# Kernel tuning notes

Hardware: AMD Instinct MI355X
Metric: run time of the kernel (lower is better)

## Reference

```python
import math
import jax, jax.numpy as jnp
import numpy as np

D_MODEL = 512
N_HEADS = 8
HD = D_MODEL // N_HEADS  # 64
RATIO = 8      # csa_compress_ratio
STRIDE = 4     # csa_compress_stride
WINDOW = 128   # csa_window_size
THETA = 10000.0


def _rope_freqs(L):
    half = HD // 2
    inv_freq = 1.0 / (THETA ** (jnp.arange(half, dtype=jnp.float32) / half))
    t = jnp.arange(L, dtype=jnp.float32)
    f = t[:, None] * inv_freq[None, :]  # [L, half]
    return jnp.cos(f), jnp.sin(f)


def _apply_rope(x, cos, sin):
    # x: [B, H, L, hd]
    half = x.shape[-1] // 2
    x1, x2 = x[..., :half], x[..., half:]
    cos = cos[None, None]
    sin = sin[None, None]
    return jnp.concatenate([x1 * cos - x2 * sin, x1 * sin + x2 * cos], axis=-1)


def setup_inputs() -> dict:
    key = jax.random.key(0)
    ks = jax.random.split(key, 9)
    B, L, D = 2, 2048, D_MODEL
    s = 0.02
    return {
        "x": jax.random.normal(ks[0], (B, L, D), dtype=jnp.float32),
        "wq": jax.random.normal(ks[1], (D, D), dtype=jnp.float32) * s,
        "wk": jax.random.normal(ks[2], (D, D), dtype=jnp.float32) * s,
        "wv": jax.random.normal(ks[3], (D, D), dtype=jnp.float32) * s,
        "wo": jax.random.normal(ks[4], (D, D), dtype=jnp.float32) * s,
        "wk_c": jax.random.normal(ks[5], (D, D), dtype=jnp.float32) * s,
        "wv_c": jax.random.normal(ks[6], (D, D), dtype=jnp.float32) * s,
        "gate_logits": jax.random.normal(ks[7], (RATIO,), dtype=jnp.float32) * s,
        "sink_logit": jnp.zeros((N_HEADS, 1), dtype=jnp.float32),
    }


def reference(x, wq, wk, wv, wo, wk_c, wv_c, gate_logits, sink_logit):
    B, L, D = x.shape
    f32 = jnp.float32

    def heads(t):  # [B,L,D] -> [B,H,L,hd]
        return t.reshape(B, L, N_HEADS, HD).transpose(0, 2, 1, 3)

    q = heads(x @ wq.T)
    k = heads(x @ wk.T)
    v = heads(x @ wv.T)

    cos, sin = _rope_freqs(L)
    q = _apply_rope(q.astype(f32), cos, sin).astype(x.dtype)
    k = _apply_rope(k.astype(f32), cos, sin).astype(x.dtype)

    # --- KV compression: strided overlapping windows, learned gate pooling ---
    n_windows = max(1, (L - RATIO) // STRIDE + 1)
    idx = jnp.clip(
        jnp.arange(RATIO)[None, :] + jnp.arange(n_windows)[:, None] * STRIDE, 0, L - 1
    )  # [Lc, ratio]
    windows = x[:, idx, :]  # [B, Lc, ratio, D]
    gate_w = jax.nn.softmax(gate_logits)
    x_c = jnp.einsum("bwrd,r->bwd", windows, gate_w)  # [B, Lc, D]
    Lc = n_windows

    k_c = x_c @ wk_c.T
    v_c = x_c @ wv_c.T
    k_c = k_c.reshape(B, Lc, N_HEADS, HD).transpose(0, 2, 1, 3)
    v_c = v_c.reshape(B, Lc, N_HEADS, HD).transpose(0, 2, 1, 3)

    scale = math.sqrt(HD)
    pos = jnp.arange(L)

    # compressed branch: causal on compressed-entry end positions
    comp_scores = jnp.einsum("bhqd,bhkd->bhqk", q, k_c) / scale  # [B,H,L,Lc]
    entry_end = jnp.arange(Lc) * STRIDE + RATIO - 1
    causal_c = pos[:, None] >= entry_end[None, :]
    comp_scores = jnp.where(causal_c[None, None], comp_scores, -jnp.inf)

    # local window branch: causal band of width WINDOW
    win_scores = jnp.einsum("bhqd,bhkd->bhqk", q, k) / scale  # [B,H,L,L]
    dist = pos[:, None] - pos[None, :]
    win_mask = (dist >= 0) & (dist < WINDOW)
    win_scores = jnp.where(win_mask[None, None], win_scores, -jnp.inf)

    sink = jnp.broadcast_to(sink_logit[None, :, None, :], (B, N_HEADS, L, 1))

    all_scores = jnp.concatenate(
        [comp_scores.astype(f32), win_scores.astype(f32), sink.astype(f32)], axis=-1
    )
    attn = jax.nn.softmax(all_scores, axis=-1).astype(x.dtype)

    w_comp = attn[..., :Lc]
    w_win = attn[..., Lc:Lc + L]
    out = jnp.einsum("bhqk,bhkd->bhqd", w_comp, v_c) + jnp.einsum(
        "bhqk,bhkd->bhqd", w_win, v
    )
    out = out.transpose(0, 2, 1, 3).reshape(B, L, D)
    return out @ wo.T
```

## Files before the change

kernel.cpp:

```cpp
#include <hip/hip_runtime.h>
#include <hip/hip_bf16.h>
#include <cmath>

#define BATCH 2
#define LSEQ 2048
#define DMODEL 512
#define NHEADS 8
#define HD 64
#define RATIO 8
#define STRIDE 4
#define WINDOW 128
#define LC 511

typedef short short8 __attribute__((ext_vector_type(8)));
typedef float floatx4 __attribute__((ext_vector_type(4)));

__device__ inline unsigned short f2bf(float f) {
  unsigned u = __float_as_uint(f);
  u += 0x7FFFu + ((u >> 16) & 1u);
  return (unsigned short)(u >> 16);
}

__device__ inline void gld_lds16(const unsigned short* g, short* l) {
  __builtin_amdgcn_global_load_lds(
      (const __attribute__((address_space(1))) unsigned int*)g,
      (__attribute__((address_space(3))) unsigned int*)l, 16, 0, 0);
}

__global__ void conv_all(const float* __restrict__ x,
                         const float* __restrict__ w0, const float* __restrict__ w1,
                         const float* __restrict__ w2, const float* __restrict__ w3,
                         const float* __restrict__ w4, const float* __restrict__ w5,
                         const float* __restrict__ gate,
                         unsigned short* __restrict__ xb,
                         unsigned short* __restrict__ wqkvb,
                         unsigned short* __restrict__ wkvcb,
                         unsigned short* __restrict__ wob,
                         unsigned short* __restrict__ xcb,
                         float2* __restrict__ cstab) {
  int idx = blockIdx.x * blockDim.x + threadIdx.x;
  if (idx < 917504) {
    const float* src;
    unsigned short* dst;
    int off;
    if (idx < 524288) {
      src = x; dst = xb; off = idx;
    } else {
      int r = idx - 524288;
      int wi = r >> 16;
      off = r & 65535;
      switch (wi) {
        case 0: src = w0; dst = wqkvb; break;
        case 1: src = w1; dst = wqkvb + 4 * 65536; break;
        case 2: src = w2; dst = wqkvb + 8 * 65536; break;
        case 3: src = w3; dst = wkvcb; break;
        case 4: src = w4; dst = wkvcb + 4 * 65536; break;
        default: src = w5; dst = wob; break;
      }
    }
    float4 v = ((const float4*)src)[off];
    ushort4 o;
    o.x = f2bf(v.x); o.y = f2bf(v.y); o.z = f2bf(v.z); o.w = f2bf(v.w);
    ((ushort4*)dst)[off] = o;
  } else if (idx < 1048320) {
    int r = idx - 917504;
    int d4 = r & 127;
    int t = r >> 7;
    int w = t % LC;
    int b = t / LC;
    float g[8];
    float m = -1e30f;
#pragma unroll
    for (int i = 0; i < 8; ++i) { g[i] = gate[i]; m = fmaxf(m, g[i]); }
    float ssum = 0.f;
#pragma unroll
    for (int i = 0; i < 8; ++i) { g[i] = __expf(g[i] - m); ssum += g[i]; }
    float inv = 1.f / ssum;
    const float* xb4 = x + ((size_t)(b * LSEQ + w * STRIDE)) * DMODEL + d4 * 4;
    float4 acc = make_float4(0.f, 0.f, 0.f, 0.f);
#pragma unroll
    for (int i = 0; i < 8; ++i) {
      float4 v = *(const float4*)(xb4 + (size_t)i * DMODEL);
      acc.x += g[i] * v.x; acc.y += g[i] * v.y;
      acc.z += g[i] * v.z; acc.w += g[i] * v.w;
    }
    ushort4 o;
    o.x = f2bf(acc.x * inv); o.y = f2bf(acc.y * inv);
    o.z = f2bf(acc.z * inv); o.w = f2bf(acc.w * inv);
    ((ushort4*)xcb)[(size_t)(b * LC + w) * 128 + d4] = o;
  } else {
    int e = idx - 1048320;
    int p = e >> 5, j = e & 31;
    float inv_freq = __expf(-(float)j * (9.210340371976184f / 32.f));
    float s, c;
    sincosf((float)p * inv_freq, &s, &c);
    cstab[e] = make_float2(c, s);
  }
}

__global__ __launch_bounds__(256) void proj_gemm(
    const unsigned short* __restrict__ xb, const unsigned short* __restrict__ xcb,
    const unsigned short* __restrict__ wqkvb, const unsigned short* __restrict__ wkvcb,
    const float2* __restrict__ cstab,
    unsigned short* __restrict__ qbuf, unsigned short* __restrict__ kbuf,
    unsigned short* __restrict__ vbuf, unsigned short* __restrict__ kcb,
    unsigned short* __restrict__ vcb) {
  __shared__ short As[128 * 64];
  __shared__ short Bs[128 * 64];
  const int tid = threadIdx.x;
  const int w = tid >> 6, l = tid & 63;
  const int lr = l & 15, lg = l >> 4;

  const int bid = blockIdx.x;
  const bool qkv = (bid < 384);
  const unsigned short* Ap;
  const unsigned short* Bp;
  int bm, bn, Am1;
  if (qkv) {
    Ap = xb; Bp = wqkvb; bm = (bid & 31) * 128; bn = (bid >> 5) * 128; Am1 = 4095;
  } else {
    int r = bid - 384;
    Ap = xcb; Bp = wkvcb; bm = (r & 7) * 128; bn = (r >> 3) * 128; Am1 = 1021;
  }
  const int wm = (w >> 1) * 64, wn = (w & 1) * 64;

  floatx4 acc[4][4];
#pragma unroll
  for (int i = 0; i < 4; ++i)
#pragma unroll
    for (int j = 0; j < 4; ++j) acc[i][j] = 0.f;

  const int trow = tid >> 3;
  const int cs = (tid & 7) ^ (trow & 7);
  size_t aoffs[4];
#pragma unroll
  for (int i = 0; i < 4; ++i) {
    int ar = bm + trow + i * 32;
    if (ar > Am1) ar = Am1;
    aoffs[i] = (size_t)ar * DMODEL + cs * 8;
  }
  const size_t boff = (size_t)(bn + trow) * DMODEL + cs * 8;
  const int ldsbase = (tid & 192) * 8;

  for (int k0 = 0; k0 < DMODEL; k0 += 64) {
    __syncthreads();
#pragma unroll
    for (int i = 0; i < 4; ++i) {
      gld_lds16(Ap + aoffs[i] + k0, As + i * 2048 + ldsbase);
      gld_lds16(Bp + boff + (size_t)i * 32 * DMODEL + k0, Bs + i * 2048 + ldsbase);
    }
    __syncthreads();

#pragma unroll
    for (int kk = 0; kk < 2; ++kk) {
      const int kc16 = kk * 4 + lg;
      short8 a[4], bf[4];
#pragma unroll
      for (int mi = 0; mi < 4; ++mi) {
        int r = wm + mi * 16 + lr;
        a[mi] = *(const short8*)&As[r * 64 + ((kc16 ^ (r & 7)) * 8)];
      }
#pragma unroll
      for (int nj = 0; nj < 4; ++nj) {
        int r = wn + nj * 16 + lr;
        bf[nj] = *(const short8*)&Bs[r * 64 + ((kc16 ^ (r & 7)) * 8)];
      }
#pragma unroll
      for (int mi = 0; mi < 4; ++mi)
#pragma unroll
        for (int nj = 0; nj < 4; ++nj)
          acc[mi][nj] = __builtin_amdgcn_mfma_f32_16x16x32_bf16(
              a[mi], bf[nj], acc[mi][nj], 0, 0, 0);
    }
  }

  if (qkv) {
    if (bn < 1024) {
      unsigned short* dst = (bn < 512) ? qbuf : kbuf;
      const int cbase = (bn + wn) & 511;
#pragma unroll
      for (int mi = 0; mi < 4; ++mi) {
#pragma unroll
        for (int i = 0; i < 4; ++i) {
          int row = bm + wm + mi * 16 + lg * 4 + i;
          int p = row & 2047;
#pragma unroll
          for (int nj = 0; nj < 2; ++nj) {
            float2 cssin = cstab[p * 32 + nj * 16 + lr];
            float a = acc[mi][nj][i], b2 = acc[mi][nj + 2][i];
            int cc = cbase + nj * 16 + lr;
            dst[(size_t)row * 512 + cc] = f2bf(a * cssin.x - b2 * cssin.y);
            dst[(size_t)row * 512 + cc + 32] = f2bf(a * cssin.y + b2 * cssin.x);
          }
        }
      }
    } else {
#pragma unroll
      for (int mi = 0; mi < 4; ++mi) {
#pragma unroll
        for (int i = 0; i < 4; ++i) {
          int row = bm + wm + mi * 16 + lg * 4 + i;
#pragma unroll
          for (int nj = 0; nj < 4; ++nj) {
            int col = bn + wn + nj * 16 + lr - 1024;
            vbuf[(size_t)row * 512 + col] = f2bf(acc[mi][nj][i]);
          }
        }
      }
    }
  } else {
    unsigned short* dst = ((bn + wn) < 512) ? kcb : vcb;
    const int cbase = (bn + wn) & 511;
#pragma unroll
    for (int mi = 0; mi < 4; ++mi) {
#pragma unroll
      for (int i = 0; i < 4; ++i) {
        int row = bm + wm + mi * 16 + lg * 4 + i;
        if (row < 1022) {
#pragma unroll
          for (int nj = 0; nj < 4; ++nj)
            dst[(size_t)row * 512 + cbase + nj * 16 + lr] = f2bf(acc[mi][nj][i]);
        }
      }
    }
  }
}

__global__ __launch_bounds__(256) void wo_gemm(
    const unsigned short* __restrict__ A, const unsigned short* __restrict__ B,
    float* __restrict__ C) {
  __shared__ short As[128 * 64];
  __shared__ short Bs[64 * 64];
  const int tid = threadIdx.x;
  const int w = tid >> 6, l = tid & 63;
  const int lr = l & 15, lg = l >> 4;
  const int bm = blockIdx.x * 128, bn = blockIdx.y * 64;
  const int wm = (w >> 1) * 64, wn = (w & 1) * 32;

  floatx4 acc[4][2];
#pragma unroll
  for (int i = 0; i < 4; ++i)
#pragma unroll
    for (int j = 0; j < 2; ++j) acc[i][j] = 0.f;

  const int trow = tid >> 3;
  const int cs = (tid & 7) ^ (trow & 7);
  const size_t aoff = (size_t)(bm + trow) * DMODEL + cs * 8;
  const size_t boff = (size_t)(bn + trow) * DMODEL + cs * 8;
  const int ldsbase = (tid & 192) * 8;

  for (int k0 = 0; k0 < DMODEL; k0 += 64) {
    __syncthreads();
#pragma unroll
    for (int i = 0; i < 4; ++i)
      gld_lds16(A + aoff + (size_t)i * 32 * DMODEL + k0, As + i * 2048 + ldsbase);
#pragma unroll
    for (int i = 0; i < 2; ++i)
      gld_lds16(B + boff + (size_t)i * 32 * DMODEL + k0, Bs + i * 2048 + ldsbase);
    __syncthreads();

#pragma unroll
    for (int kk = 0; kk < 2; ++kk) {
      const int kc16 = kk * 4 + lg;
      short8 a[4], bf[2];
#pragma unroll
      for (int mi = 0; mi < 4; ++mi) {
        int r = wm + mi * 16 + lr;
        a[mi] = *(const short8*)&As[r * 64 + ((kc16 ^ (r & 7)) * 8)];
      }
#pragma unroll
      for (int nj = 0; nj < 2; ++nj) {
        int r = wn + nj * 16 + lr;
        bf[nj] = *(const short8*)&Bs[r * 64 + ((kc16 ^ (r & 7)) * 8)];
      }
#pragma unroll
      for (int mi = 0; mi < 4; ++mi)
#pragma unroll
        for (int nj = 0; nj < 2; ++nj)
          acc[mi][nj] = __builtin_amdgcn_mfma_f32_16x16x32_bf16(
              a[mi], bf[nj], acc[mi][nj], 0, 0, 0);
    }
  }

#pragma unroll
  for (int mi = 0; mi < 4; ++mi) {
#pragma unroll
    for (int i = 0; i < 4; ++i) {
      int row = bm + wm + mi * 16 + lg * 4 + i;
#pragma unroll
      for (int nj = 0; nj < 2; ++nj)
        C[(size_t)row * 512 + bn + wn + nj * 16 + lr] = acc[mi][nj][i];
    }
  }
}

__global__ __launch_bounds__(256, 2) void attn_kernel(
    const unsigned short* __restrict__ qb, const unsigned short* __restrict__ kb,
    const unsigned short* __restrict__ vb, const unsigned short* __restrict__ kcb,
    const unsigned short* __restrict__ vcb, const float* __restrict__ sink,
    unsigned short* __restrict__ ob) {
  __shared__ short Ks[2][64][72];
  __shared__ short Vt[2][64][72];
  __shared__ short Pl[4][16][72];

  const int n = blockIdx.x;
  const int b = n >> 8;
  const int mm = n & 255;
  const int h = mm >> 5;
  int qt = mm & 31;
  if (b) qt = 31 - qt;
  const int q0 = qt * 64;
  const int tid = threadIdx.x;
  const int w = tid >> 6, l = tid & 63;
  const int lr = l & 15, lg = l >> 4;
  const int hoff = h * HD;

  short8 Qa0, Qa1;
  {
    const unsigned short* qrow =
        qb + ((size_t)(b * LSEQ + q0 + w * 16 + lr)) * DMODEL + hoff;
    Qa0 = *(const short8*)(qrow + lg * 8);
    Qa1 = *(const short8*)(qrow + 32 + lg * 8);
  }

  floatx4 Oacc[4];
#pragma unroll
  for (int f = 0; f < 4; ++f) Oacc[f] = 0.f;
  float mrow[4] = {-3.0e38f, -3.0e38f, -3.0e38f, -3.0e38f};
  float lrow[4] = {0.f, 0.f, 0.f, 0.f};

  int ncm = q0 / 4 + 15;
  if (ncm > LC) ncm = LC;
  const int ntc = (ncm + 63) >> 6;
  const int w0 = (q0 > 127) ? (q0 - 127) : 0;
  const int ntw = (q0 + 64 - w0 + 63) >> 6;
  const int ntt = ntc + ntw;

  const int skey = tid >> 2, sd = (tid & 3) * 16;
  const int vkey = (tid & 31) * 2, vd = (tid >> 5) * 8;

  short8 kreg0, kreg1, vreg0, vreg1;

  auto load_tile = [&](int tt) {
    const bool isC = (tt < ntc);
    const int tbase = isC ? tt * 64 : (w0 + (tt - ntc) * 64);
    const unsigned short* Kp = isC ? kcb : kb;
    const unsigned short* Vp = isC ? vcb : vb;
    const int rmax = isC ? (LC - 1) : (LSEQ - 1);
    const size_t brow = isC ? (size_t)(b * LC) : (size_t)(b * LSEQ);
    int kr = tbase + skey;      if (kr > rmax) kr = rmax;
    int vr0 = tbase + vkey;     if (vr0 > rmax) vr0 = rmax;
    int vr1 = tbase + vkey + 1; if (vr1 > rmax) vr1 = rmax;
    const unsigned short* src = Kp + (brow + kr) * DMODEL + hoff + sd;
    kreg0 = *(const short8*)(src);
    kreg1 = *(const short8*)(src + 8);
    vreg0 = *(const short8*)(Vp + (brow + vr0) * DMODEL + hoff + vd);
    vreg1 = *(const short8*)(Vp + (brow + vr1) * DMODEL + hoff + vd);
  };
  auto store_tile = [&](int bsel) {
    *(short8*)&Ks[bsel][skey][sd] = kreg0;
    *(short8*)&Ks[bsel][skey][sd + 8] = kreg1;
#pragma unroll
    for (int j = 0; j < 8; ++j) {
      unsigned pk = (unsigned)(unsigned short)vreg0[j] |
                    ((unsigned)(unsigned short)vreg1[j] << 16);
      *(unsigned*)&Vt[bsel][vd + j][vkey] = pk;
    }
  };

  load_tile(0);

  for (int tt = 0; tt < ntt; ++tt) {
    const int bsel = tt & 1;
    store_tile(bsel);
    if (tt + 1 < ntt) load_tile(tt + 1);
    __syncthreads();

    const bool isC = (tt < ntc);
    const int tbase = isC ? tt * 64 : (w0 + (tt - ntc) * 64);

    floatx4 S[4];
    __builtin_amdgcn_s_setprio(1);
#pragma unroll
    for (int f = 0; f < 4; ++f) {
      floatx4 acc = 0.f;
      short8 kf0 = *(const short8*)&Ks[bsel][f * 16 + lr][lg * 8];
      short8 kf1 = *(const short8*)&Ks[bsel][f * 16 + lr][32 + lg * 8];
      acc = __builtin_amdgcn_mfma_f32_16x16x32_bf16(Qa0, kf0, acc, 0, 0, 0);
      acc = __builtin_amdgcn_mfma_f32_16x16x32_bf16(Qa1, kf1, acc, 0, 0, 0);
      S[f] = acc;
    }
    __builtin_amdgcn_s_setprio(0);

    float tmax[4] = {-3.0e38f, -3.0e38f, -3.0e38f, -3.0e38f};
#pragma unroll
    for (int f = 0; f < 4; ++f) {
      const int key = tbase + f * 16 + lr;
#pragma unroll
      for (int i = 0; i < 4; ++i) {
        const int p = q0 + w * 16 + lg * 4 + i;
        bool valid;
        if (isC) valid = (key <= LC - 1) && (p >= key * 4 + 7);
        else     valid = (p >= key) && (p - key < WINDOW);
        float s = valid ? S[f][i] * 0.125f : -3.0e38f;
        S[f][i] = s;
        tmax[i] = fmaxf(tmax[i], s);
      }
    }
#pragma unroll
    for (int i = 0; i < 4; ++i) {
      tmax[i] = fmaxf(tmax[i], __shfl_xor(tmax[i], 1));
      tmax[i] = fmaxf(tmax[i], __shfl_xor(tmax[i], 2));
      tmax[i] = fmaxf(tmax[i], __shfl_xor(tmax[i], 4));
      tmax[i] = fmaxf(tmax[i], __shfl_xor(tmax[i], 8));
    }
    float r[4];
#pragma unroll
    for (int i = 0; i < 4; ++i) {
      float mn = fmaxf(mrow[i], tmax[i]);
      r[i] = __expf(mrow[i] - mn);
      mrow[i] = mn;
    }
#pragma unroll
    for (int f = 0; f < 4; ++f) {
#pragma unroll
      for (int i = 0; i < 4; ++i) Oacc[f][i] *= r[i];
    }
    float lsum[4] = {0.f, 0.f, 0.f, 0.f};
#pragma unroll
    for (int f = 0; f < 4; ++f) {
#pragma unroll
      for (int i = 0; i < 4; ++i) {
        float ee = (S[f][i] > -1.0e38f) ? __expf(S[f][i] - mrow[i]) : 0.f;
        lsum[i] += ee;
        Pl[w][lg * 4 + i][f * 16 + lr] = (short)f2bf(ee);
      }
    }
#pragma unroll
    for (int i = 0; i < 4; ++i) {
      float t = lsum[i];
      t += __shfl_xor(t, 1); t += __shfl_xor(t, 2);
      t += __shfl_xor(t, 4); t += __shfl_xor(t, 8);
      lrow[i] = lrow[i] * r[i] + t;
    }
    asm volatile("s_waitcnt lgkmcnt(0)" ::: "memory");

    __builtin_amdgcn_s_setprio(1);
#pragma unroll
    for (int c = 0; c < 2; ++c) {
      short8 Pa = *(const short8*)&Pl[w][lr][c * 32 + lg * 8];
#pragma unroll
      for (int f = 0; f < 4; ++f) {
        short8 Vf = *(const short8*)&Vt[bsel][f * 16 + lr][c * 32 + lg * 8];
        Oacc[f] = __builtin_amdgcn_mfma_f32_16x16x32_bf16(Pa, Vf, Oacc[f], 0, 0, 0);
      }
    }
    __builtin_amdgcn_s_setprio(0);
  }

  const float snk = sink[h];
  float osc[4];
#pragma unroll
  for (int i = 0; i < 4; ++i) {
    float ms = fmaxf(mrow[i], snk);
    float sc = __expf(mrow[i] - ms);
    float li = lrow[i] * sc + __expf(snk - ms);
    osc[i] = sc / li;
  }
#pragma unroll
  for (int f = 0; f < 4; ++f) {
#pragma unroll
    for (int i = 0; i < 4; ++i) {
      size_t row = (size_t)(b * LSEQ + q0 + w * 16 + lg * 4 + i);
      ob[row * DMODEL + hoff + f * 16 + lr] = f2bf(Oacc[f][i] * osc[i]);
    }
  }
}

extern "C" void kernel_launch(void* const* d_in, const int* in_sizes, int n_in,
                              void* d_out, int out_size, void* d_ws, size_t ws_size,
                              hipStream_t stream) {
  const float* x    = (const float*)d_in[0];
  const float* wq   = (const float*)d_in[1];
  const float* wk   = (const float*)d_in[2];
  const float* wv   = (const float*)d_in[3];
  const float* wo   = (const float*)d_in[4];
  const float* wkc  = (const float*)d_in[5];
  const float* wvc  = (const float*)d_in[6];
  const float* gate = (const float*)d_in[7];
  const float* sink = (const float*)d_in[8];
  float* out = (float*)d_out;

  const int BL  = BATCH * LSEQ;
  const int BLC = BATCH * LC;
  const int NX  = BATCH * LSEQ * DMODEL;
  const int NW  = DMODEL * DMODEL;

  char* wp = (char*)d_ws;
  auto carve = [&](size_t bytes) {
    char* r = wp;
    wp += (bytes + 255) & ~(size_t)255;
    return r;
  };
  unsigned short* qbuf = (unsigned short*)carve((size_t)BL * DMODEL * 2);
  unsigned short* kbuf = (unsigned short*)carve((size_t)BL * DMODEL * 2);
  unsigned short* vbuf = (unsigned short*)carve((size_t)BL * DMODEL * 2);
  unsigned short* kcb  = (unsigned short*)carve((size_t)BLC * DMODEL * 2);
  unsigned short* vcb  = (unsigned short*)carve((size_t)BLC * DMODEL * 2);
  unsigned short* xb   = (unsigned short*)carve((size_t)NX * 2);
  unsigned short* xcb  = (unsigned short*)carve((size_t)BLC * DMODEL * 2);
  unsigned short* ob   = (unsigned short*)carve((size_t)BL * DMODEL * 2);
  unsigned short* wqkvb = (unsigned short*)carve((size_t)NW * 3 * 2);
  unsigned short* wkvcb = (unsigned short*)carve((size_t)NW * 2 * 2);
  unsigned short* wob   = (unsigned short*)carve((size_t)NW * 2);
  float2* cstab = (float2*)carve((size_t)2048 * 32 * sizeof(float2));

  conv_all<<<4351, 256, 0, stream>>>(x, wq, wk, wv, wkc, wvc, wo, gate,
                                     xb, wqkvb, wkvcb, wob, xcb, cstab);

  proj_gemm<<<448, 256, 0, stream>>>(xb, xcb, wqkvb, wkvcb, cstab,
                                     qbuf, kbuf, vbuf, kcb, vcb);

  attn_kernel<<<BATCH * NHEADS * (LSEQ / 64), 256, 0, stream>>>(
      qbuf, kbuf, vbuf, kcb, vcb, sink, ob);

  wo_gemm<<<dim3(BL / 128, DMODEL / 64), 256, 0, stream>>>(ob, wob, out);
}
```

Measured before the change: 62.12 us.

## Split attention key tiles across two wave groups and merge softmax states

Doubles the attention block to 512 threads. Two groups of four waves each process alternating key tiles for the same 64 queries, each with its own double-buffered K/V in shared memory. At the end the two partial online-softmax states (O, m, l) are merged through shared memory, and the sink term is folded in during the merge. This shortens the serial per-block tile loop and raises wave-level parallelism, at the cost of more LDS, an extra merge step with barriers, and possible load imbalance when the tile count is odd.

```diff
diff --git a/kernel.cpp b/kernel.cpp
--- a/kernel.cpp
+++ b/kernel.cpp
@@ -294,14 +294,15 @@
   }
 }
 
-__global__ __launch_bounds__(256, 2) void attn_kernel(
+__global__ __launch_bounds__(512, 2) void attn_kernel(
     const unsigned short* __restrict__ qb, const unsigned short* __restrict__ kb,
     const unsigned short* __restrict__ vb, const unsigned short* __restrict__ kcb,
     const unsigned short* __restrict__ vcb, const float* __restrict__ sink,
     unsigned short* __restrict__ ob) {
-  __shared__ short Ks[2][64][72];
-  __shared__ short Vt[2][64][72];
-  __shared__ short Pl[4][16][72];
+  __shared__ short Ks[2][2][64][72];
+  __shared__ short Vt[2][2][64][72];
+  __shared__ short Pl[8][16][72];
+  __shared__ float mexm[4][16], mexl[4][16];
 
   const int n = blockIdx.x;
   const int b = n >> 8;
@@ -311,14 +312,18 @@
   if (b) qt = 31 - qt;
   const int q0 = qt * 64;
   const int tid = threadIdx.x;
-  const int w = tid >> 6, l = tid & 63;
+  const int w = tid >> 6;
+  const int grp = w >> 2;
+  const int wq = w & 3;
+  const int l = tid & 63;
   const int lr = l & 15, lg = l >> 4;
   const int hoff = h * HD;
+  const int gtid = tid & 255;
 
   short8 Qa0, Qa1;
   {
     const unsigned short* qrow =
-        qb + ((size_t)(b * LSEQ + q0 + w * 16 + lr)) * DMODEL + hoff;
+        qb + ((size_t)(b * LSEQ + q0 + wq * 16 + lr)) * DMODEL + hoff;
     Qa0 = *(const short8*)(qrow + lg * 8);
     Qa1 = *(const short8*)(qrow + 32 + lg * 8);
   }
@@ -335,9 +340,10 @@
   const int w0 = (q0 > 127) ? (q0 - 127) : 0;
   const int ntw = (q0 + 64 - w0 + 63) >> 6;
   const int ntt = ntc + ntw;
-
-  const int skey = tid >> 2, sd = (tid & 3) * 16;
-  const int vkey = (tid & 31) * 2, vd = (tid >> 5) * 8;
+  const int S = (ntt + 1) >> 1;
+
+  const int skey = gtid >> 2, sd = (gtid & 3) * 16;
+  const int vkey = (gtid & 31) * 2, vd = (gtid >> 5) * 8;
 
   short8 kreg0, kreg1, vreg0, vreg1;
 
@@ -357,38 +363,41 @@
     vreg0 = *(const short8*)(Vp + (brow + vr0) * DMODEL + hoff + vd);
     vreg1 = *(const short8*)(Vp + (brow + vr1) * DMODEL + hoff + vd);
   };
-  auto store_tile = [&](int bsel) {
-    *(short8*)&Ks[bsel][skey][sd] = kreg0;
-    *(short8*)&Ks[bsel][skey][sd + 8] = kreg1;
+  auto store_tile = [&](int par) {
+    *(short8*)&Ks[grp][par][skey][sd] = kreg0;
+    *(short8*)&Ks[grp][par][skey][sd + 8] = kreg1;
 #pragma unroll
     for (int j = 0; j < 8; ++j) {
       unsigned pk = (unsigned)(unsigned short)vreg0[j] |
                     ((unsigned)(unsigned short)vreg1[j] << 16);
-      *(unsigned*)&Vt[bsel][vd + j][vkey] = pk;
+      *(unsigned*)&Vt[grp][par][vd + j][vkey] = pk;
     }
   };
 
-  load_tile(0);
-
-  for (int tt = 0; tt < ntt; ++tt) {
-    const int bsel = tt & 1;
-    store_tile(bsel);
-    if (tt + 1 < ntt) load_tile(tt + 1);
+  load_tile(grp);
+
+  for (int s = 0; s < S; ++s) {
+    const int tt = 2 * s + grp;
+    const bool act = (tt < ntt);
+    const int par = s & 1;
+    if (act) store_tile(par);
+    if (tt + 2 < ntt) load_tile(tt + 2);
     __syncthreads();
+    if (!act) continue;
 
     const bool isC = (tt < ntc);
     const int tbase = isC ? tt * 64 : (w0 + (tt - ntc) * 64);
 
-    floatx4 S[4];
+    floatx4 S4[4];
     __builtin_amdgcn_s_setprio(1);
 #pragma unroll
     for (int f = 0; f < 4; ++f) {
       floatx4 acc = 0.f;
-      short8 kf0 = *(const short8*)&Ks[bsel][f * 16 + lr][lg * 8];
-      short8 kf1 = *(const short8*)&Ks[bsel][f * 16 + lr][32 + lg * 8];
+      short8 kf0 = *(const short8*)&Ks[grp][par][f * 16 + lr][lg * 8];
+      short8 kf1 = *(const short8*)&Ks[grp][par][f * 16 + lr][32 + lg * 8];
       acc = __builtin_amdgcn_mfma_f32_16x16x32_bf16(Qa0, kf0, acc, 0, 0, 0);
       acc = __builtin_amdgcn_mfma_f32_16x16x32_bf16(Qa1, kf1, acc, 0, 0, 0);
-      S[f] = acc;
+      S4[f] = acc;
     }
     __builtin_amdgcn_s_setprio(0);
 
@@ -398,12 +407,12 @@
       const int key = tbase + f * 16 + lr;
 #pragma unroll
       for (int i = 0; i < 4; ++i) {
-        const int p = q0 + w * 16 + lg * 4 + i;
+        const int p = q0 + wq * 16 + lg * 4 + i;
         bool valid;
         if (isC) valid = (key <= LC - 1) && (p >= key * 4 + 7);
         else     valid = (p >= key) && (p - key < WINDOW);
-        float s = valid ? S[f][i] * 0.125f : -3.0e38f;
-        S[f][i] = s;
+        float s = valid ? S4[f][i] * 0.125f : -3.0e38f;
+        S4[f][i] = s;
         tmax[i] = fmaxf(tmax[i], s);
       }
     }
@@ -431,7 +440,7 @@
     for (int f = 0; f < 4; ++f) {
 #pragma unroll
       for (int i = 0; i < 4; ++i) {
-        float ee = (S[f][i] > -1.0e38f) ? __expf(S[f][i] - mrow[i]) : 0.f;
+        float ee = (S4[f][i] > -1.0e38f) ? __expf(S4[f][i] - mrow[i]) : 0.f;
         lsum[i] += ee;
         Pl[w][lg * 4 + i][f * 16 + lr] = (short)f2bf(ee);
       }
@@ -451,28 +460,52 @@
       short8 Pa = *(const short8*)&Pl[w][lr][c * 32 + lg * 8];
 #pragma unroll
       for (int f = 0; f < 4; ++f) {
-        short8 Vf = *(const short8*)&Vt[bsel][f * 16 + lr][c * 32 + lg * 8];
+        short8 Vf = *(const short8*)&Vt[grp][par][f * 16 + lr][c * 32 + lg * 8];
         Oacc[f] = __builtin_amdgcn_mfma_f32_16x16x32_bf16(Pa, Vf, Oacc[f], 0, 0, 0);
       }
     }
     __builtin_amdgcn_s_setprio(0);
   }
 
-  const float snk = sink[h];
-  float osc[4];
-#pragma unroll
-  for (int i = 0; i < 4; ++i) {
-    float ms = fmaxf(mrow[i], snk);
-    float sc = __expf(mrow[i] - ms);
-    float li = lrow[i] * sc + __expf(snk - ms);
-    osc[i] = sc / li;
-  }
-#pragma unroll
-  for (int f = 0; f < 4; ++f) {
+  __syncthreads();
+  float* Osh = (float*)&Ks[0][0][0][0];
+  if (grp == 1) {
+#pragma unroll
+    for (int f = 0; f < 4; ++f)
+#pragma unroll
+      for (int i = 0; i < 4; ++i)
+        Osh[(wq * 16 + lg * 4 + i) * 64 + f * 16 + lr] = Oacc[f][i];
+    if (lr == 0) {
+#pragma unroll
+      for (int i = 0; i < 4; ++i) {
+        mexm[wq][lg * 4 + i] = mrow[i];
+        mexl[wq][lg * 4 + i] = lrow[i];
+      }
+    }
+  }
+  __syncthreads();
+  if (grp == 0) {
+    const float snk = sink[h];
+    float e0[4], e1[4], inv[4];
 #pragma unroll
     for (int i = 0; i < 4; ++i) {
-      size_t row = (size_t)(b * LSEQ + q0 + w * 16 + lg * 4 + i);
-      ob[row * DMODEL + hoff + f * 16 + lr] = f2bf(Oacc[f][i] * osc[i]);
+      float m1 = mexm[wq][lg * 4 + i];
+      float l1 = mexl[wq][lg * 4 + i];
+      float ms = fmaxf(fmaxf(mrow[i], m1), snk);
+      e0[i] = __expf(mrow[i] - ms);
+      e1[i] = __expf(m1 - ms);
+      float li = lrow[i] * e0[i] + l1 * e1[i] + __expf(snk - ms);
+      inv[i] = 1.f / li;
+    }
+#pragma unroll
+    for (int f = 0; f < 4; ++f) {
+#pragma unroll
+      for (int i = 0; i < 4; ++i) {
+        float o1 = Osh[(wq * 16 + lg * 4 + i) * 64 + f * 16 + lr];
+        float val = (Oacc[f][i] * e0[i] + o1 * e1[i]) * inv[i];
+        size_t row = (size_t)(b * LSEQ + q0 + wq * 16 + lg * 4 + i);
+        ob[row * DMODEL + hoff + f * 16 + lr] = f2bf(val);
+      }
     }
   }
 }
@@ -521,7 +554,7 @@
   proj_gemm<<<448, 256, 0, stream>>>(xb, xcb, wqkvb, wkvcb, cstab,
                                      qbuf, kbuf, vbuf, kcb, vcb);
 
-  attn_kernel<<<BATCH * NHEADS * (LSEQ / 64), 256, 0, stream>>>(
+  attn_kernel<<<BATCH * NHEADS * (LSEQ / 64), 512, 0, stream>>>(
       qbuf, kbuf, vbuf, kcb, vcb, sink, ob);
 
   wo_gemm<<<dim3(BL / 128, DMODEL / 64), 256, 0, stream>>>(ob, wob, out);
```

New measurement: 70.95 us. 1.14x slower.
